# Kernel optimization log

Measured on AMD Instinct MI355X. Metric: run time of the kernel, lower is better.

The kernel has to match this reference:

```python
import jax, jax.numpy as jnp
import numpy as np

EPS = 1e-6
NUM_HEADS = 16


def setup_inputs() -> dict:
    key = jax.random.key(0)
    ks = jax.random.split(key, 11)
    B, S, E = 2, 2048, 1024
    sc = 1.0 / np.sqrt(E)
    return {
        "x": jax.random.normal(ks[0], (B, S, E), dtype=jnp.float32),
        "Wq": jax.random.normal(ks[1], (E, E), dtype=jnp.float32) * sc,
        "bq": jax.random.normal(ks[2], (E,), dtype=jnp.float32) * 0.01,
        "Wk": jax.random.normal(ks[3], (E, E), dtype=jnp.float32) * sc,
        "bk": jax.random.normal(ks[4], (E,), dtype=jnp.float32) * 0.01,
        "Wv": jax.random.normal(ks[5], (E, E), dtype=jnp.float32) * sc,
        "bv": jax.random.normal(ks[6], (E,), dtype=jnp.float32) * 0.01,
        "Wp": jax.random.normal(ks[7], (E, E), dtype=jnp.float32) * sc,
        "bp": jax.random.normal(ks[8], (E,), dtype=jnp.float32) * 0.01,
        "gain": jax.random.uniform(ks[9], (E,), dtype=jnp.float32),
        "beta": jax.random.normal(ks[10], (E,), dtype=jnp.float32),
    }


def _layer_norm(x, gain, beta):
    # torch: (x - mean) / (std + eps) * gain + bias, std with Bessel correction
    mean = jnp.mean(x, axis=-1, keepdims=True)
    std = jnp.std(x, axis=-1, keepdims=True, ddof=1)
    return (x - mean) / (std + EPS) * gain + beta


def reference(x, Wq, bq, Wk, bk, Wv, bv, Wp, bp, gain, beta):
    B, S, E = x.shape
    H = NUM_HEADS
    D = E // H
    # QKV projections, split heads: [B,S,E] -> [B,H,S,D]
    def heads(y):
        return y.reshape(B, S, H, D).transpose(0, 2, 1, 3)
    q = heads(x @ Wq + bq)
    k = heads(x @ Wk + bk)
    v = heads(x @ Wv + bv)
    # scores [B,H,S,S], mask=None path (no causal mask applied in forward)
    scores = jnp.einsum("bhid,bhjd->bhij", q, k) / jnp.sqrt(jnp.float32(D))
    attn = jax.nn.softmax(scores, axis=-1)  # dropout is identity at eval
    y = jnp.einsum("bhij,bhjd->bhid", attn, v)
    y = y.transpose(0, 2, 1, 3).reshape(B, S, E)
    return _layer_norm(y @ Wp + bp, gain, beta)
```

## Files before the change

kernel.cpp:

```cpp
#include <hip/hip_runtime.h>
#include <hip/hip_bf16.h>
#include <math.h>

constexpr int Bc = 2;
constexpr int Sc = 2048;
constexpr int Ec = 1024;
constexpr int Hc = 16;
constexpr int Dc = 64;

typedef __attribute__((ext_vector_type(8))) short short8;
typedef __attribute__((ext_vector_type(4))) short short4v;
typedef __attribute__((ext_vector_type(2))) int int2v;
typedef __attribute__((ext_vector_type(4))) int int4v;
typedef __attribute__((ext_vector_type(4))) float f32x4;

__device__ inline unsigned short f2bf(float x) {
    __hip_bfloat16 h = __float2bfloat16(x);
    return *reinterpret_cast<unsigned short*>(&h);
}

__device__ inline float bf2f(unsigned short u) {
    unsigned int v = (unsigned int)u << 16;
    return __builtin_bit_cast(float, v);
}

__device__ inline f32x4 mfma16(short8 a, short8 b, f32x4 c) {
    return __builtin_amdgcn_mfma_f32_16x16x32_bf16(a, b, c, 0, 0, 0);
}

__device__ inline float exp2_fast(float x) {
    float r;
    asm("v_exp_f32 %0, %1" : "=v"(r) : "v"(x));
    return r;
}

__device__ inline int cvt_pk_bf16(float lo, float hi) {
    int r;
    asm("v_cvt_pk_bf16_f32 %0, %1, %2" : "=v"(r) : "v"(lo), "v"(hi));
    return r;
}

__device__ inline void gload_lds16(const unsigned short* gsrc, unsigned short* ldst) {
    __builtin_amdgcn_global_load_lds(
        (const __attribute__((address_space(1))) unsigned int*)(const void*)gsrc,
        (__attribute__((address_space(3))) unsigned int*)(void*)ldst,
        16, 0, 0);
}

__global__ __launch_bounds__(256) void prep_kernel(
    const float* __restrict__ X, unsigned short* __restrict__ Xb,
    const float* __restrict__ W0, const float* __restrict__ W1,
    const float* __restrict__ W2, const float* __restrict__ W3,
    unsigned short* __restrict__ T0, unsigned short* __restrict__ T1,
    unsigned short* __restrict__ T2, unsigned short* __restrict__ T3)
{
    __shared__ unsigned short Ls[64][72];
    const int bid = blockIdx.x, t = threadIdx.x;
    if (bid < 2048) {
        int i = bid * 256 + t;
        const float4* src = (const float4*)(X + (size_t)i * 8);
        float4 a = src[0], b = src[1];
        short8 o;
        o[0] = f2bf(a.x); o[1] = f2bf(a.y); o[2] = f2bf(a.z); o[3] = f2bf(a.w);
        o[4] = f2bf(b.x); o[5] = f2bf(b.y); o[6] = f2bf(b.z); o[7] = f2bf(b.w);
        *(short8*)(Xb + (size_t)i * 8) = o;
        return;
    }
    const int tt = bid - 2048;
    const float* W; unsigned short* T;
    switch (tt >> 8) {
        case 0: W = W0; T = T0; break;
        case 1: W = W1; T = T1; break;
        case 2: W = W2; T = T2; break;
        default: W = W3; T = T3; break;
    }
    const int rem = tt & 255;
    const int n0 = (rem & 15) * 64, k0 = (rem >> 4) * 64;
    {
        int k = t >> 2, nb = (t & 3) * 16;
        const float* src = W + (size_t)(k0 + k) * Ec + n0 + nb;
#pragma unroll
        for (int j = 0; j < 16; ++j) Ls[k][nb + j] = f2bf(src[j]);
    }
    __syncthreads();
    {
        int n = t >> 2, kb = (t & 3) * 16;
        short8 o0, o1;
#pragma unroll
        for (int j = 0; j < 8; ++j) { o0[j] = Ls[kb + j][n]; o1[j] = Ls[kb + 8 + j][n]; }
        unsigned short* dst = T + (size_t)(n0 + n) * Ec + k0 + kb;
        *(short8*)dst = o0;
        *(short8*)(dst + 8) = o1;
    }
}

constexpr int BM = 128, BK = 64;

template<int BNt>
__device__ __forceinline__ void gemm_core_t(
    const unsigned short* __restrict__ A, const unsigned short* __restrict__ Bt,
    const float* __restrict__ bias, float* __restrict__ Cf,
    unsigned short* __restrict__ Cb, int M, int N, int K, int mode, float oscale)
{
    constexpr int NW = BNt / 32;
    constexpr int WN = BNt / 2;
    constexpr int CH = (BM + BNt) / 8;
    constexpr int PW = CH / 4;
    __shared__ unsigned short lds[2][(BM + BNt) * BK];
    const int tid = threadIdx.x, lane = tid & 63, wid = tid >> 6;
    const int c16 = lane & 15, g = lane >> 4;
    const int wr = wid >> 1, wc = wid & 1;
    const int row0 = blockIdx.y * BM, col0 = blockIdx.x * BNt;

    const int rsub = lane >> 3;
    const int colE = ((lane & 7) ^ rsub) * 8;

    f32x4 acc[4][NW] = {};

    auto stage = [&](int buf, int k0) {
        unsigned short* Ab = &lds[buf][0];
        unsigned short* Bb = &lds[buf][BM * BK];
#pragma unroll
        for (int i = 0; i < PW; ++i) {
            int c = wid * PW + i;
            if (c < 16) {
                const unsigned short* src = A + (size_t)(row0 + c * 8 + rsub) * K + k0 + colE;
                gload_lds16(src, Ab + c * 512);
            } else {
                int c2 = c - 16;
                const unsigned short* src = Bt + (size_t)(col0 + c2 * 8 + rsub) * K + k0 + colE;
                gload_lds16(src, Bb + c2 * 512);
            }
        }
    };

    stage(0, 0);
    __syncthreads();
    int cur = 0;
    const int NT = K / BK;
    for (int t = 0; t < NT; ++t) {
        if (t + 1 < NT) stage(cur ^ 1, (t + 1) * BK);
        const unsigned short* Ab = &lds[cur][0];
        const unsigned short* Bb = &lds[cur][BM * BK];
#pragma unroll
        for (int kk = 0; kk < 2; ++kk) {
            const int cb = ((kk * 64 + g * 16) ^ ((c16 & 7) << 4)) >> 1;
            short8 af[4], bfr[NW];
#pragma unroll
            for (int m = 0; m < 4; ++m) {
                int row = wr * 64 + m * 16 + c16;
                af[m] = *(const short8*)(Ab + row * BK + cb);
            }
#pragma unroll
            for (int n = 0; n < NW; ++n) {
                int row = wc * WN + n * 16 + c16;
                bfr[n] = *(const short8*)(Bb + row * BK + cb);
            }
#pragma unroll
            for (int m = 0; m < 4; ++m)
#pragma unroll
                for (int n = 0; n < NW; ++n)
                    acc[m][n] = mfma16(af[m], bfr[n], acc[m][n]);
        }
        __syncthreads();
        cur ^= 1;
    }

#pragma unroll
    for (int m = 0; m < 4; ++m) {
#pragma unroll
        for (int n = 0; n < NW; ++n) {
            int gc = col0 + wc * WN + n * 16 + c16;
            float bi = bias[gc];
            if (mode == 2) {
                int h = gc >> 6, d = gc & (Dc - 1);
                int s0 = row0 + wr * 64 + m * 16 + g * 4;
                int a = (s0 >> 2) & 7;
                int sp = (s0 & ~31) + ((a & 3) << 3) + ((a >> 2) << 2);
                int b = s0 >> 11, s = sp & (Sc - 1);
                short4v pk;
#pragma unroll
                for (int r = 0; r < 4; ++r)
                    pk[r] = (short)f2bf((acc[m][n][r] + bi) * oscale);
                *(short4v*)&Cb[(((size_t)b * Hc + h) * Dc + d) * Sc + s] = pk;
            } else {
#pragma unroll
                for (int r = 0; r < 4; ++r) {
                    int gr = row0 + wr * 64 + m * 16 + g * 4 + r;
                    float v = (acc[m][n][r] + bi) * oscale;
                    if (mode == 0) {
                        Cf[(size_t)gr * N + gc] = v;
                    } else if (mode == 3) {
                        Cb[(size_t)gr * N + gc] = f2bf(v);
                    } else {
                        int b = gr >> 11, s = gr & (Sc - 1);
                        int h = gc >> 6, d = gc & (Dc - 1);
                        Cb[(((size_t)b * Hc + h) * Sc + s) * Dc + d] = f2bf(v);
                    }
                }
            }
        }
    }
}

__global__ __launch_bounds__(256) void gemm_mfma_kernel(
    const unsigned short* __restrict__ A, const unsigned short* __restrict__ Bt,
    const float* __restrict__ bias, unsigned short* __restrict__ Cb,
    int M, int N, int K)
{
    gemm_core_t<64>(A, Bt, bias, nullptr, Cb, M, N, K, 3, 1.0f);
}

__global__ __launch_bounds__(256) void qkv_gemm_kernel(
    const unsigned short* __restrict__ A,
    const unsigned short* __restrict__ WqT, const unsigned short* __restrict__ WkT,
    const unsigned short* __restrict__ WvT,
    const float* __restrict__ bq, const float* __restrict__ bk,
    const float* __restrict__ bv,
    unsigned short* __restrict__ Qb, unsigned short* __restrict__ Kb,
    unsigned short* __restrict__ Vt, int M, int N, int K, float sl2e)
{
    if (blockIdx.z == 0)      gemm_core_t<128>(A, WqT, bq, nullptr, Qb, M, N, K, 1, sl2e);
    else if (blockIdx.z == 1) gemm_core_t<128>(A, WkT, bk, nullptr, Kb, M, N, K, 1, 1.0f);
    else                      gemm_core_t<128>(A, WvT, bv, nullptr, Vt, M, N, K, 2, 1.0f);
}

__global__ __launch_bounds__(256) void attn_mfma_kernel(
    const unsigned short* __restrict__ Q, const unsigned short* __restrict__ K,
    const unsigned short* __restrict__ Vt, unsigned short* __restrict__ Y)
{
    __shared__ __align__(16) unsigned short lds[2][2][64 * 64];

    const int tid  = threadIdx.x;
    const int lane = tid & 63, wid = tid >> 6;
    const int g = lane >> 4, c16 = lane & 15;
    const int bh = blockIdx.x;
    const int qw = blockIdx.y * 128 + wid * 32;
    const size_t base = (size_t)bh * Sc * Dc;

    short8 bq[2][2];
#pragma unroll
    for (int u = 0; u < 2; ++u) {
        const unsigned short* Qp = Q + base + (size_t)(qw + u * 16 + c16) * Dc;
        bq[u][0] = *(const short8*)(Qp + g * 8);
        bq[u][1] = *(const short8*)(Qp + 32 + g * 8);
    }

    const int rsub = lane >> 3;
    const int srcoffE = 8 * ((lane & 7) ^ rsub);
    const int row0g = (wid * 2 + 0) * 8 + rsub;
    const int row1g = (wid * 2 + 1) * 8 + rsub;

    const unsigned short* kg0 = K  + base + (size_t)row0g * Dc + srcoffE;
    const unsigned short* kg1 = K  + base + (size_t)row1g * Dc + srcoffE;
    const unsigned short* vg0 = Vt + base + (size_t)row0g * Sc + srcoffE;
    const unsigned short* vg1 = Vt + base + (size_t)row1g * Sc + srcoffE;

    f32x4 o[2][4] = {};
    f32x4 acc_ps[2] = {};
    const short8 ones8 = {(short)0x3F80, (short)0x3F80, (short)0x3F80, (short)0x3F80,
                          (short)0x3F80, (short)0x3F80, (short)0x3F80, (short)0x3F80};

    auto stage = [&](unsigned short* kbuf, unsigned short* vbuf) {
        gload_lds16(kg0, kbuf + (wid * 2 + 0) * 512);
        gload_lds16(kg1, kbuf + (wid * 2 + 1) * 512);
        gload_lds16(vg0, vbuf + (wid * 2 + 0) * 512);
        gload_lds16(vg1, vbuf + (wid * 2 + 1) * 512);
        kg0 += 64 * Dc; kg1 += 64 * Dc;
        vg0 += 64;      vg1 += 64;
    };

    const int sw = (c16 & 7) << 4;

    auto compute = [&](const unsigned short* kbuf, const unsigned short* vbuf) {
        const char* kbc = (const char*)kbuf;
        const char* vbc = (const char*)vbuf;

        f32x4 c[2][4];
        __builtin_amdgcn_s_setprio(1);
#pragma unroll
        for (int ct = 0; ct < 4; ++ct) {
            const int kr = ct * 16 + c16;
            short8 alo = *(const short8*)(kbc + kr * 128 + ((16 * g) ^ sw));
            short8 ahi = *(const short8*)(kbc + kr * 128 + ((64 + 16 * g) ^ sw));
            f32x4 z0 = {}, z1 = {};
            z0 = mfma16(alo, bq[0][0], z0);
            c[0][ct] = mfma16(ahi, bq[0][1], z0);
            z1 = mfma16(alo, bq[1][0], z1);
            c[1][ct] = mfma16(ahi, bq[1][1], z1);
        }
        __builtin_amdgcn_s_setprio(0);

        int4v p32[2][2];
#pragma unroll
        for (int u = 0; u < 2; ++u) {
#pragma unroll
            for (int ct = 0; ct < 4; ++ct) {
                float p0 = exp2_fast(c[u][ct][0]);
                float p1 = exp2_fast(c[u][ct][1]);
                float p2 = exp2_fast(c[u][ct][2]);
                float p3 = exp2_fast(c[u][ct][3]);
                p32[u][ct >> 1][(ct & 1) * 2 + 0] = cvt_pk_bf16(p0, p1);
                p32[u][ct >> 1][(ct & 1) * 2 + 1] = cvt_pk_bf16(p2, p3);
            }
        }

        __builtin_amdgcn_s_setprio(1);
#pragma unroll
        for (int w = 0; w < 2; ++w) {
            short8 pb0 = __builtin_bit_cast(short8, p32[0][w]);
            short8 pb1 = __builtin_bit_cast(short8, p32[1][w]);
            acc_ps[0] = mfma16(ones8, pb0, acc_ps[0]);
            acc_ps[1] = mfma16(ones8, pb1, acc_ps[1]);
#pragma unroll
            for (int dt = 0; dt < 4; ++dt) {
                const int drow = dt * 16 + c16;
                short8 va = *(const short8*)(vbc + drow * 128 + ((w * 64 + 16 * g) ^ sw));
                o[0][dt] = mfma16(va, pb0, o[0][dt]);
                o[1][dt] = mfma16(va, pb1, o[1][dt]);
            }
        }
        __builtin_amdgcn_s_setprio(0);
    };

    unsigned short* k0b = &lds[0][0][0]; unsigned short* v0b = &lds[0][1][0];
    unsigned short* k1b = &lds[1][0][0]; unsigned short* v1b = &lds[1][1][0];

    constexpr int NT = Sc / 64;
    stage(k0b, v0b);
    for (int kt = 0; kt < NT; kt += 2) {
        asm volatile("s_waitcnt vmcnt(0)" ::: "memory");
        __builtin_amdgcn_s_barrier();
        __builtin_amdgcn_sched_barrier(0);
        if (kt + 1 < NT) stage(k1b, v1b);
        compute(k0b, v0b);
        asm volatile("s_waitcnt vmcnt(0)" ::: "memory");
        __builtin_amdgcn_s_barrier();
        __builtin_amdgcn_sched_barrier(0);
        if (kt + 2 < NT) stage(k0b, v0b);
        compute(k1b, v1b);
    }

    const int b = bh >> 4, h = bh & (Hc - 1);
#pragma unroll
    for (int u = 0; u < 2; ++u) {
        const float inv = 1.f / acc_ps[u][0];
        const int qg = qw + u * 16 + c16;
        unsigned short* yrow = Y + ((size_t)b * Sc + qg) * Ec + h * Dc;
#pragma unroll
        for (int dt = 0; dt < 4; ++dt) {
            int2v wv;
            wv[0] = cvt_pk_bf16(o[u][dt][0] * inv, o[u][dt][1] * inv);
            wv[1] = cvt_pk_bf16(o[u][dt][2] * inv, o[u][dt][3] * inv);
            *(int2v*)&yrow[dt * 16 + g * 4] = wv;
        }
    }
}

__global__ __launch_bounds__(256) void ln_kernel(
    const unsigned short* __restrict__ Z, const float* __restrict__ gain,
    const float* __restrict__ beta, float* __restrict__ out)
{
    __shared__ float red0[4];
    __shared__ float red1[4];
    const int row = blockIdx.x;
    const int t = threadIdx.x;
    short4v zv = *(const short4v*)(Z + (size_t)row * Ec + t * 4);
    float v0 = bf2f((unsigned short)zv[0]);
    float v1 = bf2f((unsigned short)zv[1]);
    float v2 = bf2f((unsigned short)zv[2]);
    float v3 = bf2f((unsigned short)zv[3]);

    float s = (v0 + v1) + (v2 + v3);
#pragma unroll
    for (int off = 32; off > 0; off >>= 1) s += __shfl_down(s, off);
    if ((t & 63) == 0) red0[t >> 6] = s;
    __syncthreads();
    float mean = (red0[0] + red0[1] + red0[2] + red0[3]) * (1.0f / Ec);

    float dx = v0 - mean; float vs = dx * dx;
    dx = v1 - mean; vs += dx * dx;
    dx = v2 - mean; vs += dx * dx;
    dx = v3 - mean; vs += dx * dx;
#pragma unroll
    for (int off = 32; off > 0; off >>= 1) vs += __shfl_down(vs, off);
    if ((t & 63) == 0) red1[t >> 6] = vs;
    __syncthreads();
    float var = (red1[0] + red1[1] + red1[2] + red1[3]) * (1.0f / (Ec - 1));
    float inv = 1.0f / (sqrtf(var) + 1e-6f);

    float4 gn = ((const float4*)gain)[t];
    float4 bb = ((const float4*)beta)[t];
    float4 o;
    o.x = (v0 - mean) * inv * gn.x + bb.x;
    o.y = (v1 - mean) * inv * gn.y + bb.y;
    o.z = (v2 - mean) * inv * gn.z + bb.z;
    o.w = (v3 - mean) * inv * gn.w + bb.w;
    ((float4*)(out + (size_t)row * Ec))[t] = o;
}

extern "C" void kernel_launch(void* const* d_in, const int* in_sizes, int n_in,
                              void* d_out, int out_size, void* d_ws, size_t ws_size,
                              hipStream_t stream)
{
    const float* x    = (const float*)d_in[0];
    const float* Wq   = (const float*)d_in[1];
    const float* bq   = (const float*)d_in[2];
    const float* Wk   = (const float*)d_in[3];
    const float* bk   = (const float*)d_in[4];
    const float* Wv   = (const float*)d_in[5];
    const float* bv   = (const float*)d_in[6];
    const float* Wp   = (const float*)d_in[7];
    const float* bp   = (const float*)d_in[8];
    const float* gain = (const float*)d_in[9];
    const float* beta = (const float*)d_in[10];

    const int M = Bc * Sc;
    const size_t MK  = (size_t)M * Ec;
    const size_t EE  = (size_t)Ec * Ec;

    unsigned short* xb  = (unsigned short*)d_ws;
    unsigned short* wqt = xb + MK;
    unsigned short* wkt = wqt + EE;
    unsigned short* wvt = wkt + EE;
    unsigned short* wpt = wvt + EE;
    unsigned short* qb  = wpt + EE;
    unsigned short* kb  = qb + MK;
    unsigned short* vt  = kb + MK;
    unsigned short* yb  = vt + MK;

    unsigned short* zb = qb;

    const float sl2e = 0.125f * 1.44269504f;

    prep_kernel<<<3072, 256, 0, stream>>>(x, xb, Wq, Wk, Wv, Wp, wqt, wkt, wvt, wpt);

    dim3 qkv_grid(Ec / 128, M / BM, 3);
    qkv_gemm_kernel<<<qkv_grid, 256, 0, stream>>>(
        xb, wqt, wkt, wvt, bq, bk, bv, qb, kb, vt, M, Ec, Ec, sl2e);

    dim3 attn_grid(Bc * Hc, Sc / 128);
    attn_mfma_kernel<<<attn_grid, 256, 0, stream>>>(qb, kb, vt, yb);

    dim3 proj_grid(Ec / 64, M / BM);
    gemm_mfma_kernel<<<proj_grid, 256, 0, stream>>>(yb, wpt, bp, zb, M, Ec, Ec);

    ln_kernel<<<M, 256, 0, stream>>>(zb, gain, beta, (float*)d_out);
}
```

Baseline: 116.1 us.

## Use per-wave private V buffers and direct global K loads, drop block barriers

Each wave now stages its own full V tile into a private double-buffered LDS region. K fragments are loaded straight from global memory into registers instead of being shared through LDS. This removes the block-wide barriers between pipeline stages. In exchange, each wave redundantly fetches K and V, quadrupling global/cache traffic per block. LDS use also grows substantially, which may cut occupancy.

```diff
diff --git a/kernel.cpp b/kernel.cpp
--- a/kernel.cpp
+++ b/kernel.cpp
@@ -229,7 +229,7 @@
     const unsigned short* __restrict__ Q, const unsigned short* __restrict__ K,
     const unsigned short* __restrict__ Vt, unsigned short* __restrict__ Y)
 {
-    __shared__ __align__(16) unsigned short lds[2][2][64 * 64];
+    __shared__ __align__(16) unsigned short vlds[4][2][64 * 64];
 
     const int tid  = threadIdx.x;
     const int lane = tid & 63, wid = tid >> 6;
@@ -248,41 +248,33 @@
 
     const int rsub = lane >> 3;
     const int srcoffE = 8 * ((lane & 7) ^ rsub);
-    const int row0g = (wid * 2 + 0) * 8 + rsub;
-    const int row1g = (wid * 2 + 1) * 8 + rsub;
-
-    const unsigned short* kg0 = K  + base + (size_t)row0g * Dc + srcoffE;
-    const unsigned short* kg1 = K  + base + (size_t)row1g * Dc + srcoffE;
-    const unsigned short* vg0 = Vt + base + (size_t)row0g * Sc + srcoffE;
-    const unsigned short* vg1 = Vt + base + (size_t)row1g * Sc + srcoffE;
+    const unsigned short* vgb = Vt + base + (size_t)rsub * Sc + srcoffE;
+
+    const unsigned short* kg = K + base + (size_t)c16 * Dc + 8 * g;
 
     f32x4 o[2][4] = {};
     f32x4 acc_ps[2] = {};
     const short8 ones8 = {(short)0x3F80, (short)0x3F80, (short)0x3F80, (short)0x3F80,
                           (short)0x3F80, (short)0x3F80, (short)0x3F80, (short)0x3F80};
 
-    auto stage = [&](unsigned short* kbuf, unsigned short* vbuf) {
-        gload_lds16(kg0, kbuf + (wid * 2 + 0) * 512);
-        gload_lds16(kg1, kbuf + (wid * 2 + 1) * 512);
-        gload_lds16(vg0, vbuf + (wid * 2 + 0) * 512);
-        gload_lds16(vg1, vbuf + (wid * 2 + 1) * 512);
-        kg0 += 64 * Dc; kg1 += 64 * Dc;
-        vg0 += 64;      vg1 += 64;
+    auto stageV = [&](unsigned short* buf, int kt) {
+#pragma unroll
+        for (int i = 0; i < 8; ++i)
+            gload_lds16(vgb + (size_t)i * 8 * Sc + kt * 64, buf + i * 512);
     };
 
     const int sw = (c16 & 7) << 4;
 
-    auto compute = [&](const unsigned short* kbuf, const unsigned short* vbuf) {
-        const char* kbc = (const char*)kbuf;
+    auto compute = [&](const unsigned short* vbuf, int kt) {
         const char* vbc = (const char*)vbuf;
 
         f32x4 c[2][4];
         __builtin_amdgcn_s_setprio(1);
 #pragma unroll
         for (int ct = 0; ct < 4; ++ct) {
-            const int kr = ct * 16 + c16;
-            short8 alo = *(const short8*)(kbc + kr * 128 + ((16 * g) ^ sw));
-            short8 ahi = *(const short8*)(kbc + kr * 128 + ((64 + 16 * g) ^ sw));
+            const unsigned short* kro = kg + (size_t)(kt * 64 + ct * 16) * Dc;
+            short8 alo = *(const short8*)kro;
+            short8 ahi = *(const short8*)(kro + 32);
             f32x4 z0 = {}, z1 = {};
             z0 = mfma16(alo, bq[0][0], z0);
             c[0][ct] = mfma16(ahi, bq[0][1], z0);
@@ -323,22 +315,20 @@
         __builtin_amdgcn_s_setprio(0);
     };
 
-    unsigned short* k0b = &lds[0][0][0]; unsigned short* v0b = &lds[0][1][0];
-    unsigned short* k1b = &lds[1][0][0]; unsigned short* v1b = &lds[1][1][0];
+    unsigned short* b0 = &vlds[wid][0][0];
+    unsigned short* b1 = &vlds[wid][1][0];
 
     constexpr int NT = Sc / 64;
-    stage(k0b, v0b);
+    stageV(b0, 0);
     for (int kt = 0; kt < NT; kt += 2) {
         asm volatile("s_waitcnt vmcnt(0)" ::: "memory");
-        __builtin_amdgcn_s_barrier();
         __builtin_amdgcn_sched_barrier(0);
-        if (kt + 1 < NT) stage(k1b, v1b);
-        compute(k0b, v0b);
+        if (kt + 1 < NT) stageV(b1, kt + 1);
+        compute(b0, kt);
         asm volatile("s_waitcnt vmcnt(0)" ::: "memory");
-        __builtin_amdgcn_s_barrier();
         __builtin_amdgcn_sched_barrier(0);
-        if (kt + 2 < NT) stage(k0b, v0b);
-        compute(k1b, v1b);
+        if (kt + 2 < NT) stageV(b0, kt + 2);
+        compute(b1, kt + 1);
     }
 
     const int b = bh >> 4, h = bh & (Hc - 1);
```

Result: slower. 152.3 us (+31.1%).

## Software-pipeline attention with 4-stage LDS ring and QK/softmax-PV interleave

Applied to the files above, without the earlier changes.

Raises the K/V LDS ring from two to four buffers so loads run two tiles ahead, waiting only on older loads (vmcnt 4). The loop is split into a QK step and a softmax-PV step, so the QK MFMAs for tile k+1 are issued before the exp and PV work for tile k. This overlaps exp/convert ALU work with matrix ops and hides global load latency. In exchange it doubles LDS use to 64KB per block, which may lower occupancy, and holds a second set of score registers.

```diff
diff --git a/kernel.cpp b/kernel.cpp
--- a/kernel.cpp
+++ b/kernel.cpp
@@ -229,7 +229,7 @@
     const unsigned short* __restrict__ Q, const unsigned short* __restrict__ K,
     const unsigned short* __restrict__ Vt, unsigned short* __restrict__ Y)
 {
-    __shared__ __align__(16) unsigned short lds[2][2][64 * 64];
+    __shared__ __align__(16) unsigned short lds[4][2][64 * 64];
 
     const int tid  = threadIdx.x;
     const int lane = tid & 63, wid = tid >> 6;
@@ -258,6 +258,7 @@
 
     f32x4 o[2][4] = {};
     f32x4 acc_ps[2] = {};
+    f32x4 cA[2][4], cB[2][4];
     const short8 ones8 = {(short)0x3F80, (short)0x3F80, (short)0x3F80, (short)0x3F80,
                           (short)0x3F80, (short)0x3F80, (short)0x3F80, (short)0x3F80};
 
@@ -272,11 +273,8 @@
 
     const int sw = (c16 & 7) << 4;
 
-    auto compute = [&](const unsigned short* kbuf, const unsigned short* vbuf) {
+    auto qk = [&](const unsigned short* kbuf, f32x4 (&c)[2][4]) {
         const char* kbc = (const char*)kbuf;
-        const char* vbc = (const char*)vbuf;
-
-        f32x4 c[2][4];
         __builtin_amdgcn_s_setprio(1);
 #pragma unroll
         for (int ct = 0; ct < 4; ++ct) {
@@ -290,7 +288,10 @@
             c[1][ct] = mfma16(ahi, bq[1][1], z1);
         }
         __builtin_amdgcn_s_setprio(0);
-
+    };
+
+    auto smpv = [&](const f32x4 (&c)[2][4], const unsigned short* vbuf) {
+        const char* vbc = (const char*)vbuf;
         int4v p32[2][2];
 #pragma unroll
         for (int u = 0; u < 2; ++u) {
@@ -304,7 +305,6 @@
                 p32[u][ct >> 1][(ct & 1) * 2 + 1] = cvt_pk_bf16(p2, p3);
             }
         }
-
         __builtin_amdgcn_s_setprio(1);
 #pragma unroll
         for (int w = 0; w < 2; ++w) {
@@ -323,23 +323,51 @@
         __builtin_amdgcn_s_setprio(0);
     };
 
-    unsigned short* k0b = &lds[0][0][0]; unsigned short* v0b = &lds[0][1][0];
-    unsigned short* k1b = &lds[1][0][0]; unsigned short* v1b = &lds[1][1][0];
-
-    constexpr int NT = Sc / 64;
-    stage(k0b, v0b);
-    for (int kt = 0; kt < NT; kt += 2) {
-        asm volatile("s_waitcnt vmcnt(0)" ::: "memory");
-        __builtin_amdgcn_s_barrier();
-        __builtin_amdgcn_sched_barrier(0);
-        if (kt + 1 < NT) stage(k1b, v1b);
-        compute(k0b, v0b);
-        asm volatile("s_waitcnt vmcnt(0)" ::: "memory");
-        __builtin_amdgcn_s_barrier();
-        __builtin_amdgcn_sched_barrier(0);
-        if (kt + 2 < NT) stage(k0b, v0b);
-        compute(k1b, v1b);
-    }
+    unsigned short* kB[4] = {&lds[0][0][0], &lds[1][0][0], &lds[2][0][0], &lds[3][0][0]};
+    unsigned short* vB[4] = {&lds[0][1][0], &lds[1][1][0], &lds[2][1][0], &lds[3][1][0]};
+
+#define WAITBAR(N)                                        \
+    asm volatile("s_waitcnt vmcnt(" #N ")" ::: "memory"); \
+    __builtin_amdgcn_s_barrier();                         \
+    __builtin_amdgcn_sched_barrier(0);
+
+    stage(kB[0], vB[0]);
+    stage(kB[1], vB[1]);
+    WAITBAR(4)
+    stage(kB[2], vB[2]);
+    qk(kB[0], cA);
+
+#pragma unroll 1
+    for (int kt = 1; kt <= 25; kt += 4) {
+        WAITBAR(4)
+        stage(kB[3], vB[3]);
+        qk(kB[1], cB);
+        smpv(cA, vB[0]);
+        WAITBAR(4)
+        stage(kB[0], vB[0]);
+        qk(kB[2], cA);
+        smpv(cB, vB[1]);
+        WAITBAR(4)
+        stage(kB[1], vB[1]);
+        qk(kB[3], cB);
+        smpv(cA, vB[2]);
+        WAITBAR(4)
+        stage(kB[2], vB[2]);
+        qk(kB[0], cA);
+        smpv(cB, vB[3]);
+    }
+    WAITBAR(4)
+    stage(kB[3], vB[3]);
+    qk(kB[1], cB);
+    smpv(cA, vB[0]);
+    WAITBAR(4)
+    qk(kB[2], cA);
+    smpv(cB, vB[1]);
+    WAITBAR(0)
+    qk(kB[3], cB);
+    smpv(cA, vB[2]);
+    smpv(cB, vB[3]);
+#undef WAITBAR
 
     const int b = bh >> 4, h = bh & (Hc - 1);
 #pragma unroll
```

Measured after the change: 113.5 us. 2.2% less time.
